# Kernel tuning notes

Hardware: AMD Instinct MI355X
Metric: run time of the kernel (lower is better)

The kernel has to match this reference:

```python
import jax, jax.numpy as jnp
import numpy as np

B, H, F, T = 256, 1024, 512, 128  # batch, state_size, num_feature, num_predict

def setup_inputs() -> dict:
    key = jax.random.key(0)
    ks = jax.random.split(key, 8)
    s = 1.0 / np.sqrt(H)
    return {
        "x0": jax.random.normal(ks[0], (B, H), jnp.float32),
        "h0": jax.random.normal(ks[1], (B, H), jnp.float32),
        "c0": jax.random.normal(ks[2], (B, H), jnp.float32),
        "W": jax.random.uniform(ks[3], (H, 4 * H), jnp.float32, -s, s),   # input kernel (i,f,g,o)
        "U": jax.random.uniform(ks[4], (H, 4 * H), jnp.float32, -s, s),   # recurrent kernel
        "b": jnp.zeros((4 * H,), jnp.float32),
        "Wd": jax.random.uniform(ks[5], (H, F), jnp.float32, -s, s),      # Dense emission
        "bd": jnp.zeros((F,), jnp.float32),
    }

def _lstm_scan(x0, h0, c0, W, U, b):
    def step(carry, _):
        x, h, c = carry
        z = x @ W + h @ U + b                      # [B, 4H], Keras gate order i,f,g,o
        i, f, g, o = jnp.split(z, 4, axis=-1)
        c_new = jax.nn.sigmoid(f) * c + jax.nn.sigmoid(i) * jnp.tanh(g)
        h_new = jax.nn.sigmoid(o) * jnp.tanh(c_new)
        return (h_new, h_new, c_new), h_new       # output feeds back as next input
    (_, _, _), outs = jax.lax.scan(step, (x0, h0, c0), None, length=T)
    return outs                                    # [T, B, H]

def reference(x0, h0, c0, W, U, b, Wd, bd):
    outs = _lstm_scan(x0, h0, c0, W, U, b)         # [T, B, H]
    seq = jnp.transpose(outs, (1, 0, 2))           # [B, T, H]
    return seq @ Wd + bd                           # [B, T, F]
```

## Files before the change

### kernel.cpp

```cpp
#include <hip/hip_runtime.h>
#include <cstddef>
#include <cstdint>

typedef unsigned short ushort_t;
typedef __attribute__((ext_vector_type(8))) short bf16x8;
typedef __attribute__((ext_vector_type(4))) float f32x4;

#define Bb 256
#define Hh 1024
#define Ff 512
#define Tt 128

__device__ __forceinline__ ushort_t f2bf(float f) {
    unsigned int u = __float_as_uint(f);
    unsigned int r = (u + 0x7FFFu + ((u >> 16) & 1u)) >> 16;
    return (ushort_t)r;
}
__device__ __forceinline__ float sigf(float x)  { return 1.0f / (1.0f + __expf(-x)); }
__device__ __forceinline__ float tanhf_(float x){ return 2.0f / (1.0f + __expf(-2.0f * x)) - 1.0f; }

__global__ void swz(const float* __restrict__ s0, const float* __restrict__ s1,
                    ushort_t* __restrict__ dst, int K, int N, int mode, int total)
{
    int KB = K >> 5;
    for (int idx = blockIdx.x * blockDim.x + threadIdx.x; idx < total;
         idx += gridDim.x * blockDim.x) {
        int blk   = idx >> 9;
        int lane  = (idx >> 3) & 63;
        int j     = idx & 7;
        int ntile = blk / KB;
        int kstep = blk - ntile * KB;
        int k = (kstep << 5) + ((lane >> 4) << 3) + j;
        int n;
        if (mode == 2) n = (ntile << 4) + (lane & 15);
        else           n = ((ntile & 3) << 10) + ((ntile >> 2) << 4) + (lane & 15);
        float v;
        if (mode == 0)      v = s0[(size_t)k * N + n] + s1[(size_t)k * N + n];
        else if (mode == 1) v = (k < 1024) ? s0[(size_t)k * N + n]
                                           : s1[(size_t)(k - 1024) * N + n];
        else                v = s0[(size_t)k * N + n];
        dst[idx] = f2bf(v);
    }
}

__global__ void mk_a0(const float* __restrict__ x0, const float* __restrict__ h0,
                      ushort_t* __restrict__ a0)
{
    int idx = blockIdx.x * blockDim.x + threadIdx.x;
    if (idx >= Bb * 2048) return;
    int r = idx >> 11, k = idx & 2047;
    float v = (k < 1024) ? x0[r * 1024 + k] : h0[r * 1024 + k - 1024];
    a0[idx] = f2bf(v);
}

__global__ void zero_bar(int* bar) {
    int i = blockIdx.x * blockDim.x + threadIdx.x;
    if (i < 1024) bar[i] = 0;
}


__global__ __launch_bounds__(256) void lstm_step(
    const ushort_t* __restrict__ Ap, int K,
    const ushort_t* __restrict__ Bw,
    const float* cin, float* cout,
    ushort_t* __restrict__ seqt,
    const float* __restrict__ bias)
{
    __shared__ __align__(16) ushort_t lA[32 * 512];
    __shared__ __align__(16) ushort_t lB[32 * 512];

    const int tid = threadIdx.x, w = tid >> 6, lane = tid & 63;
    const int id = blockIdx.x;
    const int ntg = ((id & 7) << 3) | (id >> 5);
    const int bt  = (id >> 3) & 3;
    const int r0 = bt << 6, hb = ntg << 4;
    const int wr = w >> 1, wc = w & 1;
    const int KB = K >> 5;

    f32x4 acc[2][2];
    #pragma unroll
    for (int m = 0; m < 2; ++m)
        #pragma unroll
        for (int n = 0; n < 2; ++n) acc[m][n] = (f32x4){0.f, 0.f, 0.f, 0.f};

    const int kp = tid & 31;
    const int q_a = kp & 3, kk_a = kp >> 2;

    for (int kc = 0; kc < K; kc += 256) {
        bf16x8 va[8];
        #pragma unroll
        for (int i = 0; i < 8; ++i) {
            int row = (i << 3) + (tid >> 5);
            va[i] = *(const bf16x8*)(Ap + (size_t)(r0 + row) * K + kc + (kp << 3));
        }
        bf16x8 vb[8];
        #pragma unroll
        for (int i = 0; i < 8; ++i)
            vb[i] = *(const bf16x8*)(Bw +
                ((((size_t)((ntg << 2) + w)) * KB + (kc >> 5) + i) << 9) + (lane << 3));
        #pragma unroll
        for (int i = 0; i < 8; ++i) {
            int row = (i << 3) + (tid >> 5);
            int msub = row >> 4, mm = row & 15;
            int pos = (q_a << 4) | (mm ^ (((kk_a << 2) + q_a) & 15));
            *(bf16x8*)&lA[((((kk_a << 2) + msub) << 6) + pos) << 3] = va[i];
        }
        #pragma unroll
        for (int i = 0; i < 8; ++i)
            *(bf16x8*)&lB[(((i << 2) + w) << 9) + (lane << 3)] = vb[i];
        __syncthreads();

        #pragma unroll
        for (int kk = 0; kk < 8; ++kk) {
            const int qq = lane >> 4, mm = lane & 15;
            const int pos = (qq << 4) | (mm ^ (((kk << 2) + qq) & 15));
            bf16x8 af[2], bfr[2];
            #pragma unroll
            for (int m = 0; m < 2; ++m)
                af[m] = *(const bf16x8*)&lA[((((kk << 2) + (wr << 1) + m) << 6) + pos) << 3];
            #pragma unroll
            for (int n = 0; n < 2; ++n)
                bfr[n] = *(const bf16x8*)&lB[((((kk << 2) + (wc << 1) + n) << 6) + lane) << 3];
            #pragma unroll
            for (int m = 0; m < 2; ++m)
                #pragma unroll
                for (int n = 0; n < 2; ++n)
                    acc[m][n] = __builtin_amdgcn_mfma_f32_16x16x32_bf16(
                        af[m], bfr[n], acc[m][n], 0, 0, 0);
        }
        __syncthreads();
    }

    float* lZ = (float*)lA;
    {
        int q = lane >> 4, nl = lane & 15;
        #pragma unroll
        for (int m = 0; m < 2; ++m)
            #pragma unroll
            for (int n = 0; n < 2; ++n)
                #pragma unroll
                for (int r = 0; r < 4; ++r)
                    lZ[((wr << 5) + (m << 4) + (q << 2) + r) * 68 +
                       (wc << 5) + (n << 4) + nl] = acc[m][n][r];
    }
    __syncthreads();

    #pragma unroll
    for (int i = 0; i < 4; ++i) {
        int idx = (i << 8) + tid;
        int row = idx >> 4, u = idx & 15;
        float zi = lZ[row * 68 +      u] + bias[       hb + u];
        float zf = lZ[row * 68 + 16 + u] + bias[1024 + hb + u];
        float zg = lZ[row * 68 + 32 + u] + bias[2048 + hb + u];
        float zo = lZ[row * 68 + 48 + u] + bias[3072 + hb + u];
        size_t cidx = (size_t)(r0 + row) * Hh + hb + u;
        float cp = cin[cidx];
        float cn = sigf(zf) * cp + sigf(zi) * tanhf_(zg);
        cout[cidx] = cn;
        seqt[cidx] = f2bf(sigf(zo) * tanhf_(cn));
    }
}

__global__ __launch_bounds__(256, 1) void lstm_scan(
    ushort_t* __restrict__ seq,
    const ushort_t* __restrict__ Msum,
    const float* __restrict__ bias,
    const float* __restrict__ cin,
    int* __restrict__ bar)
{
    __shared__ __align__(16) ushort_t lA[2][4096];

    const int tid = threadIdx.x, w = tid >> 6, lane = tid & 63;
    const int id = blockIdx.x;
    const int g  = id & 7;
    const int s  = id >> 3;
    const int r0 = g << 5;
    const int hb = s << 5;
    int* const barw = &bar[g << 5];

    bf16x8 Brg[2][32];
    #pragma unroll
    for (int n = 0; n < 2; ++n) {
        const int ntl = (w << 1) + n;
        const int gnt = (((s << 1) + (ntl >> 2)) << 2) + (ntl & 3);
        const ushort_t* bp = Msum + (((size_t)gnt << 5) << 9) + (lane << 3);
        #pragma unroll
        for (int ks = 0; ks < 32; ++ks)
            Brg[n][ks] = *(const bf16x8*)(bp + ((size_t)ks << 9));
    }

    const int grow = tid >> 3, gu4 = (tid & 7) << 2;
    float c_reg[4], bi[4], bfv[4], bgv[4], bo[4];
    #pragma unroll
    for (int j = 0; j < 4; ++j) {
        int u = gu4 + j;
        c_reg[j] = cin[(size_t)(r0 + grow) * Hh + hb + u];
        bi[j]  = bias[       hb + u];
        bfv[j] = bias[1024 + hb + u];
        bgv[j] = bias[2048 + hb + u];
        bo[j]  = bias[3072 + hb + u];
    }

    float* lZ = (float*)lA;

    const int kp  = tid & 15;
    const int q_a = kp & 3, kk_a = kp >> 2;
    const int mm_s  = tid >> 4;
    const int pos_s = (q_a << 4) | (mm_s ^ (((kk_a << 2) + q_a) & 15));
    const int lw0   = (((kk_a << 1) << 6) | pos_s) << 3;
    const size_t ga0 = (size_t)(r0 + mm_s) * Hh + (kp << 3);

    #pragma unroll 1
    for (int t = 1; t < Tt; ++t) {
        const ushort_t* Ap = seq + ((size_t)(t - 1) << 18) + ga0;

        f32x4 acc[2][2];
        #pragma unroll
        for (int m = 0; m < 2; ++m)
            #pragma unroll
            for (int n = 0; n < 2; ++n) acc[m][n] = (f32x4){0.f, 0.f, 0.f, 0.f};

        bf16x8 rA[2][2];
        #pragma unroll
        for (int i = 0; i < 2; ++i)
            rA[0][i] = *(const bf16x8*)(Ap + (i << 14));
        #pragma unroll
        for (int i = 0; i < 2; ++i)
            *(bf16x8*)&lA[0][lw0 + (i << 9)] = rA[0][i];
        #pragma unroll
        for (int i = 0; i < 2; ++i)
            rA[1][i] = *(const bf16x8*)(Ap + (i << 14) + 128);
        __syncthreads();

        #pragma unroll
        for (int kc = 0; kc < 8; ++kc) {
            if (kc < 7) {
                const int sb = (kc + 1) & 1;
                #pragma unroll
                for (int i = 0; i < 2; ++i)
                    *(bf16x8*)&lA[sb][lw0 + (i << 9)] = rA[sb][i];
            }
            if (kc < 6) {
                const int sb = kc & 1;
                #pragma unroll
                for (int i = 0; i < 2; ++i)
                    rA[sb][i] = *(const bf16x8*)(Ap + (i << 14) + ((kc + 2) << 7));
            }
            const ushort_t* lAc = lA[kc & 1];
            const int qq = lane >> 4, mr = lane & 15;
            #pragma unroll
            for (int kk = 0; kk < 4; ++kk) {
                const int pos = (qq << 4) | (mr ^ (((kk << 2) + qq) & 15));
                const int ks = (kc << 2) + kk;
                bf16x8 af0 = *(const bf16x8*)&lAc[((((kk << 1) + 0) << 6) | pos) << 3];
                bf16x8 af1 = *(const bf16x8*)&lAc[((((kk << 1) + 1) << 6) | pos) << 3];
                acc[0][0] = __builtin_amdgcn_mfma_f32_16x16x32_bf16(af0, Brg[0][ks], acc[0][0], 0, 0, 0);
                acc[0][1] = __builtin_amdgcn_mfma_f32_16x16x32_bf16(af0, Brg[1][ks], acc[0][1], 0, 0, 0);
                acc[1][0] = __builtin_amdgcn_mfma_f32_16x16x32_bf16(af1, Brg[0][ks], acc[1][0], 0, 0, 0);
                acc[1][1] = __builtin_amdgcn_mfma_f32_16x16x32_bf16(af1, Brg[1][ks], acc[1][1], 0, 0, 0);
            }
            __syncthreads();
        }

        {
            const int q = lane >> 4, nl = lane & 15;
            #pragma unroll
            for (int m = 0; m < 2; ++m)
                #pragma unroll
                for (int n = 0; n < 2; ++n)
                    #pragma unroll
                    for (int r = 0; r < 4; ++r) {
                        int row = (m << 4) + (q << 2) + r;
                        int col = (((w << 1) + n) << 4) + nl;
                        lZ[(row << 7) + ((col + row * 5) & 127)] = acc[m][n][r];
                    }
        }
        __syncthreads();

        {
            const int rb5 = grow * 5;
            unsigned long long pk = 0;
            #pragma unroll
            for (int j = 0; j < 4; ++j) {
                int u = gu4 + j;
                int cb = ((u >> 4) << 6) + (u & 15);
                float zi = lZ[(grow << 7) + ((cb      + rb5) & 127)] + bi[j];
                float zf = lZ[(grow << 7) + ((cb + 16 + rb5) & 127)] + bfv[j];
                float zg = lZ[(grow << 7) + ((cb + 32 + rb5) & 127)] + bgv[j];
                float zo = lZ[(grow << 7) + ((cb + 48 + rb5) & 127)] + bo[j];
                float cn = sigf(zf) * c_reg[j] + sigf(zi) * tanhf_(zg);
                c_reg[j] = cn;
                pk |= (unsigned long long)f2bf(sigf(zo) * tanhf_(cn)) << (j << 4);
            }
            __hip_atomic_exchange(
                (unsigned long long*)&seq[((size_t)t << 18) +
                                          (size_t)(r0 + grow) * Hh + hb + gu4],
                pk, __ATOMIC_RELAXED, __HIP_MEMORY_SCOPE_AGENT);
        }

        if (t < Tt - 1) {
            __syncthreads();
            if (tid == 0) {
                __hip_atomic_fetch_add(barw, 1, __ATOMIC_RELAXED,
                                       __HIP_MEMORY_SCOPE_AGENT);
                int guard = 0;
                while (__hip_atomic_fetch_add(barw, 0, __ATOMIC_RELAXED,
                                              __HIP_MEMORY_SCOPE_AGENT) < (t << 5)
                       && ++guard < 30000)
                    __builtin_amdgcn_s_sleep(2);
            }
            __syncthreads();
        }
    }
}

__global__ __launch_bounds__(256) void emit(
    const ushort_t* __restrict__ seq,
    const ushort_t* __restrict__ Wsw,
    const float* __restrict__ bd,
    float* __restrict__ out)
{
    __shared__ __align__(16) ushort_t lA[2 * 8 * 64 * 8];
    __shared__ __align__(16) ushort_t lB[2 * 8 * 64 * 8];
    const int tid = threadIdx.x, w = tid >> 6, lane = tid & 63;
    const int id = blockIdx.x;
    const int rt = ((id >> 5) << 3) | (id & 7);
    const int ct = (id >> 3) & 3;
    const int r0 = rt << 7, f0 = ct << 7;
    const int wr = w >> 1, wc = w & 1;

    f32x4 acc[4][4];
    #pragma unroll
    for (int m = 0; m < 4; ++m)
        #pragma unroll
        for (int n = 0; n < 4; ++n) acc[m][n] = (f32x4){0.f, 0.f, 0.f, 0.f};

    for (int kc = 0; kc < Hh; kc += 64) {
        #pragma unroll
        for (int i = 0; i < 4; ++i) {
            int p = (i << 8) + tid;
            int row = p >> 3, kpp = p & 7;
            bf16x8 v = *(const bf16x8*)(seq + (size_t)(r0 + row) * Hh + kc + (kpp << 3));
            int kk = kpp >> 2, q = kpp & 3, msub = row >> 4, mm = row & 15;
            int pos = (q << 4) | (mm ^ (((kk << 2) + q) & 15));
            *(bf16x8*)&lA[((((kk << 3) + msub) << 6) + pos) << 3] = v;
        }
        #pragma unroll
        for (int i = 0; i < 4; ++i) {
            int d = (i << 8) + tid;
            int kk = d >> 9, csub = (d >> 6) & 7, ln = d & 63;
            int nt = (ct << 3) + csub;
            bf16x8 v = *(const bf16x8*)(Wsw + (((size_t)(nt * 32 + (kc >> 5) + kk)) << 9) + (ln << 3));
            *(bf16x8*)&lB[d << 3] = v;
        }
        __syncthreads();
        const int qq = lane >> 4, mm = lane & 15;
        #pragma unroll
        for (int kk = 0; kk < 2; ++kk) {
            const int pos = (qq << 4) | (mm ^ (((kk << 2) + qq) & 15));
            bf16x8 af[4], bfr[4];
            #pragma unroll
            for (int m = 0; m < 4; ++m)
                af[m] = *(const bf16x8*)&lA[((((kk << 3) + (wr << 2) + m) << 6) + pos) << 3];
            #pragma unroll
            for (int n = 0; n < 4; ++n)
                bfr[n] = *(const bf16x8*)&lB[((((kk << 3) + (wc << 2) + n) << 6) + lane) << 3];
            #pragma unroll
            for (int m = 0; m < 4; ++m)
                #pragma unroll
                for (int n = 0; n < 4; ++n)
                    acc[m][n] = __builtin_amdgcn_mfma_f32_16x16x32_bf16(
                        af[m], bfr[n], acc[m][n], 0, 0, 0);
        }
        __syncthreads();
    }

    int q = lane >> 4, nl = lane & 15;
    float bdv[4];
    #pragma unroll
    for (int n = 0; n < 4; ++n) bdv[n] = bd[f0 + (wc << 6) + (n << 4) + nl];
    #pragma unroll
    for (int m = 0; m < 4; ++m)
        #pragma unroll
        for (int r = 0; r < 4; ++r) {
            int grow2 = r0 + (wr << 6) + (m << 4) + (q << 2) + r;
            int tt = grow2 >> 8, bb = grow2 & 255;
            float* op = out + ((size_t)((bb << 7) + tt) << 9);
            #pragma unroll
            for (int n = 0; n < 4; ++n)
                op[f0 + (wc << 6) + (n << 4) + nl] = acc[m][n][r] + bdv[n];
        }
}

extern "C" void kernel_launch(void* const* d_in, const int* in_sizes, int n_in,
                              void* d_out, int out_size, void* d_ws, size_t ws_size,
                              hipStream_t stream)
{
    const float* x0 = (const float*)d_in[0];
    const float* h0 = (const float*)d_in[1];
    const float* c0 = (const float*)d_in[2];
    const float* W  = (const float*)d_in[3];
    const float* U  = (const float*)d_in[4];
    const float* b  = (const float*)d_in[5];
    const float* Wd = (const float*)d_in[6];
    const float* bd = (const float*)d_in[7];
    float* out = (float*)d_out;

    const size_t OFF_MCAT = 0;
    const size_t OFF_MSUM = 16777216;
    const size_t OFF_WSW  = 25165824;
    const size_t OFF_A0   = 26214400;
    const size_t OFF_SEQ  = 27262976;
    const size_t OFF_BAR  = 94371840;
    const size_t WS_NEED  = 94375936;
    if (ws_size < WS_NEED) return;

    char* ws = (char*)d_ws;
    ushort_t* Mcat = (ushort_t*)(ws + OFF_MCAT);
    ushort_t* Msum = (ushort_t*)(ws + OFF_MSUM);
    ushort_t* Wsw  = (ushort_t*)(ws + OFF_WSW);
    ushort_t* A0   = (ushort_t*)(ws + OFF_A0);
    ushort_t* seq  = (ushort_t*)(ws + OFF_SEQ);
    int*      bar  = (int*)(ws + OFF_BAR);
    float* cws = out;

    zero_bar<<<4, 256, 0, stream>>>(bar);
    mk_a0<<<2048, 256, 0, stream>>>(x0, h0, A0);
    swz<<<4096, 256, 0, stream>>>(W, U, Mcat, 2048, 4096, 1, 2048 * 4096);
    swz<<<2048, 256, 0, stream>>>(W, U, Msum, 1024, 4096, 0, 1024 * 4096);
    swz<<<512, 256, 0, stream>>>(Wd, nullptr, Wsw, 1024, 512, 2, 1024 * 512);

    lstm_step<<<256, 256, 0, stream>>>(A0, 2048, Mcat, c0, cws, seq, b);
    lstm_scan<<<256, 256, 0, stream>>>(seq, Msum, b, cws, bar);

    emit<<<1024, 256, 0, stream>>>(seq, Wsw, bd, out);
}
```

Baseline: 833.0 us.

## Split LSTM step GEMM over K across warps and load the A tile in one pass

Reorganizes the persistent LSTM scan kernel so the four warps split the K dimension in two halves and the N dimension in two halves. Each warp holds 4x16 B fragments in registers, and the whole 32x1024 A tile is loaded into LDS at once instead of through a double-buffered 8-chunk pipeline. This removes the eight per-chunk __syncthreads inside the step. The two K-half partial sums go to separate LDS buffers and are added in the gate epilogue. The spin-wait sleep is also shortened. In exchange, LDS use grows, the global loads are no longer overlapped with the MFMAs, and the epilogue does extra reads and adds.

```diff
diff --git a/kernel.cpp b/kernel.cpp
--- a/kernel.cpp
+++ b/kernel.cpp
@@ -168,7 +168,8 @@
     const float* __restrict__ cin,
     int* __restrict__ bar)
 {
-    __shared__ __align__(16) ushort_t lA[2][4096];
+    __shared__ __align__(16) ushort_t lA[2][16384];
+    __shared__ __align__(16) float    lZp[2][4608];
 
     const int tid = threadIdx.x, w = tid >> 6, lane = tid & 63;
     const int id = blockIdx.x;
@@ -177,16 +178,16 @@
     const int r0 = g << 5;
     const int hb = s << 5;
     int* const barw = &bar[g << 5];
-
-    bf16x8 Brg[2][32];
-    #pragma unroll
-    for (int n = 0; n < 2; ++n) {
-        const int ntl = (w << 1) + n;
-        const int gnt = (((s << 1) + (ntl >> 2)) << 2) + (ntl & 3);
-        const ushort_t* bp = Msum + (((size_t)gnt << 5) << 9) + (lane << 3);
-        #pragma unroll
-        for (int ks = 0; ks < 32; ++ks)
-            Brg[n][ks] = *(const bf16x8*)(bp + ((size_t)ks << 9));
+    const int kw = w >> 1, nw = w & 1;
+
+    bf16x8 Brg[4][16];
+    #pragma unroll
+    for (int G = 0; G < 4; ++G) {
+        const int gnt = (((s << 1) + nw) << 2) + G;
+        const ushort_t* bp = Msum + (((size_t)(gnt << 5) + (kw << 4)) << 9) + (lane << 3);
+        #pragma unroll
+        for (int kl = 0; kl < 16; ++kl)
+            Brg[G][kl] = *(const bf16x8*)(bp + ((size_t)kl << 9));
     }
 
     const int grow = tid >> 3, gu4 = (tid & 7) << 2;
@@ -201,93 +202,66 @@
         bo[j]  = bias[3072 + hb + u];
     }
 
-    float* lZ = (float*)lA;
-
-    const int kp  = tid & 15;
-    const int q_a = kp & 3, kk_a = kp >> 2;
-    const int mm_s  = tid >> 4;
-    const int pos_s = (q_a << 4) | (mm_s ^ (((kk_a << 2) + q_a) & 15));
-    const int lw0   = (((kk_a << 1) << 6) | pos_s) << 3;
-    const size_t ga0 = (size_t)(r0 + mm_s) * Hh + (kp << 3);
+    const int kl_s = lane >> 2, q_s = lane & 3;
+    const size_t gbase = (size_t)(r0 + (nw << 4)) * Hh + (kw << 9) + (lane << 3);
+    const int qq = lane >> 4, mml = lane & 15;
 
     #pragma unroll 1
     for (int t = 1; t < Tt; ++t) {
-        const ushort_t* Ap = seq + ((size_t)(t - 1) << 18) + ga0;
-
-        f32x4 acc[2][2];
+        const ushort_t* Ap = seq + ((size_t)(t - 1) << 18) + gbase;
+
+        #pragma unroll
+        for (int half = 0; half < 2; ++half) {
+            bf16x8 rA[8];
+            #pragma unroll
+            for (int i = 0; i < 8; ++i)
+                rA[i] = *(const bf16x8*)(Ap + ((size_t)((half << 3) + i) << 10));
+            #pragma unroll
+            for (int i = 0; i < 8; ++i) {
+                int mm = (half << 3) + i;
+                int pos = (q_s << 4) | (mm ^ (((kl_s << 2) + q_s) & 15));
+                *(bf16x8*)&lA[kw][((((kl_s << 1) + nw) << 6) | pos) << 3] = rA[i];
+            }
+        }
+        __syncthreads();
+
+        f32x4 acc[2][4];
         #pragma unroll
         for (int m = 0; m < 2; ++m)
             #pragma unroll
-            for (int n = 0; n < 2; ++n) acc[m][n] = (f32x4){0.f, 0.f, 0.f, 0.f};
-
-        bf16x8 rA[2][2];
-        #pragma unroll
-        for (int i = 0; i < 2; ++i)
-            rA[0][i] = *(const bf16x8*)(Ap + (i << 14));
-        #pragma unroll
-        for (int i = 0; i < 2; ++i)
-            *(bf16x8*)&lA[0][lw0 + (i << 9)] = rA[0][i];
-        #pragma unroll
-        for (int i = 0; i < 2; ++i)
-            rA[1][i] = *(const bf16x8*)(Ap + (i << 14) + 128);
-        __syncthreads();
-
-        #pragma unroll
-        for (int kc = 0; kc < 8; ++kc) {
-            if (kc < 7) {
-                const int sb = (kc + 1) & 1;
-                #pragma unroll
-                for (int i = 0; i < 2; ++i)
-                    *(bf16x8*)&lA[sb][lw0 + (i << 9)] = rA[sb][i];
+            for (int G = 0; G < 4; ++G) acc[m][G] = (f32x4){0.f, 0.f, 0.f, 0.f};
+
+        #pragma unroll
+        for (int kl = 0; kl < 16; ++kl) {
+            const int pos = (qq << 4) | (mml ^ (((kl << 2) + qq) & 15));
+            bf16x8 af0 = *(const bf16x8*)&lA[kw][((((kl << 1) + 0) << 6) | pos) << 3];
+            bf16x8 af1 = *(const bf16x8*)&lA[kw][((((kl << 1) + 1) << 6) | pos) << 3];
+            #pragma unroll
+            for (int G = 0; G < 4; ++G) {
+                acc[0][G] = __builtin_amdgcn_mfma_f32_16x16x32_bf16(af0, Brg[G][kl], acc[0][G], 0, 0, 0);
+                acc[1][G] = __builtin_amdgcn_mfma_f32_16x16x32_bf16(af1, Brg[G][kl], acc[1][G], 0, 0, 0);
             }
-            if (kc < 6) {
-                const int sb = kc & 1;
-                #pragma unroll
-                for (int i = 0; i < 2; ++i)
-                    rA[sb][i] = *(const bf16x8*)(Ap + (i << 14) + ((kc + 2) << 7));
+        }
+
+        #pragma unroll
+        for (int m = 0; m < 2; ++m)
+            #pragma unroll
+            for (int G = 0; G < 4; ++G) {
+                int col = (nw << 6) + (G << 4) + mml;
+                *(f32x4*)&lZp[kw][col * 36 + (m << 4) + (qq << 2)] = acc[m][G];
             }
-            const ushort_t* lAc = lA[kc & 1];
-            const int qq = lane >> 4, mr = lane & 15;
-            #pragma unroll
-            for (int kk = 0; kk < 4; ++kk) {
-                const int pos = (qq << 4) | (mr ^ (((kk << 2) + qq) & 15));
-                const int ks = (kc << 2) + kk;
-                bf16x8 af0 = *(const bf16x8*)&lAc[((((kk << 1) + 0) << 6) | pos) << 3];
-                bf16x8 af1 = *(const bf16x8*)&lAc[((((kk << 1) + 1) << 6) | pos) << 3];
-                acc[0][0] = __builtin_amdgcn_mfma_f32_16x16x32_bf16(af0, Brg[0][ks], acc[0][0], 0, 0, 0);
-                acc[0][1] = __builtin_amdgcn_mfma_f32_16x16x32_bf16(af0, Brg[1][ks], acc[0][1], 0, 0, 0);
-                acc[1][0] = __builtin_amdgcn_mfma_f32_16x16x32_bf16(af1, Brg[0][ks], acc[1][0], 0, 0, 0);
-                acc[1][1] = __builtin_amdgcn_mfma_f32_16x16x32_bf16(af1, Brg[1][ks], acc[1][1], 0, 0, 0);
-            }
-            __syncthreads();
-        }
+        __syncthreads();
 
         {
-            const int q = lane >> 4, nl = lane & 15;
-            #pragma unroll
-            for (int m = 0; m < 2; ++m)
-                #pragma unroll
-                for (int n = 0; n < 2; ++n)
-                    #pragma unroll
-                    for (int r = 0; r < 4; ++r) {
-                        int row = (m << 4) + (q << 2) + r;
-                        int col = (((w << 1) + n) << 4) + nl;
-                        lZ[(row << 7) + ((col + row * 5) & 127)] = acc[m][n][r];
-                    }
-        }
-        __syncthreads();
-
-        {
-            const int rb5 = grow * 5;
             unsigned long long pk = 0;
             #pragma unroll
             for (int j = 0; j < 4; ++j) {
                 int u = gu4 + j;
                 int cb = ((u >> 4) << 6) + (u & 15);
-                float zi = lZ[(grow << 7) + ((cb      + rb5) & 127)] + bi[j];
-                float zf = lZ[(grow << 7) + ((cb + 16 + rb5) & 127)] + bfv[j];
-                float zg = lZ[(grow << 7) + ((cb + 32 + rb5) & 127)] + bgv[j];
-                float zo = lZ[(grow << 7) + ((cb + 48 + rb5) & 127)] + bo[j];
+                float zi = lZp[0][(cb     ) * 36 + grow] + lZp[1][(cb     ) * 36 + grow] + bi[j];
+                float zf = lZp[0][(cb + 16) * 36 + grow] + lZp[1][(cb + 16) * 36 + grow] + bfv[j];
+                float zg = lZp[0][(cb + 32) * 36 + grow] + lZp[1][(cb + 32) * 36 + grow] + bgv[j];
+                float zo = lZp[0][(cb + 48) * 36 + grow] + lZp[1][(cb + 48) * 36 + grow] + bo[j];
                 float cn = sigf(zf) * c_reg[j] + sigf(zi) * tanhf_(zg);
                 c_reg[j] = cn;
                 pk |= (unsigned long long)f2bf(sigf(zo) * tanhf_(cn)) << (j << 4);
@@ -307,7 +281,7 @@
                 while (__hip_atomic_fetch_add(barw, 0, __ATOMIC_RELAXED,
                                               __HIP_MEMORY_SCOPE_AGENT) < (t << 5)
                        && ++guard < 30000)
-                    __builtin_amdgcn_s_sleep(2);
+                    __builtin_amdgcn_s_sleep(1);
             }
             __syncthreads();
         }
```

Result: slower. 1.168 ms (+40.2%).
